# Optimization experiments

Measured on AMD Instinct MI355X. Metric: run time of the kernel, lower is better.

Reference implementation:

```python
import jax, jax.numpy as jnp
import numpy as np

B, C_IN, N = 8, 3, 32768
C_OUT, K, E = 128, 4, 4194304
TOTAL = B * N
BN_EPS = 1e-5


def setup_inputs() -> dict:
    key = jax.random.key(0)
    ks = jax.random.split(key, 6)
    return {
        "x": jax.random.normal(ks[0], (B, C_IN, N), dtype=jnp.float32),
        "edge_index": jax.random.randint(ks[1], (2, E), 0, TOTAL, dtype=jnp.int32),
        "edge_weight": jax.random.uniform(ks[2], (E,), dtype=jnp.float32),
        # ChebConv parameters: one (in, out) weight per Chebyshev order, plus bias
        "weight": jax.random.normal(ks[3], (K, C_IN, C_OUT), dtype=jnp.float32) * 0.1,
        "bias": jax.random.normal(ks[4], (C_OUT,), dtype=jnp.float32) * 0.01,
        # BatchNorm1d affine params
        "gamma": jnp.ones((C_OUT,), dtype=jnp.float32),
        "beta": jnp.zeros((C_OUT,), dtype=jnp.float32),
    }


def reference(x, edge_index, edge_weight, weight, bias, gamma, beta):
    b, f, n = x.shape
    total = b * n
    # (B, F, N) -> (B*N, F)
    h = x.transpose(0, 2, 1).reshape(total, f)

    src, dst = edge_index[0], edge_index[1]
    # remove_self_loops: zero self-loop weights (diagonal of scaled Laplacian is 0)
    w = jnp.where(src == dst, 0.0, edge_weight)
    # sym-normalized Laplacian, scaled by 2/lambda_max with lambda_max=2 (PyG default),
    # then self-loops added with -1 cancel the +I diagonal -> L_hat = -D^-1/2 A D^-1/2
    deg = jax.ops.segment_sum(w, src, num_segments=total)
    dis = jnp.where(deg > 0, jax.lax.rsqrt(jnp.maximum(deg, 1e-12)), 0.0)
    norm_w = -dis[src] * w * dis[dst]  # (E,)

    def prop(t):  # y[i] = sum_j L_hat[i, j] t[j]
        return jax.ops.segment_sum(norm_w[:, None] * t[src], dst, num_segments=total)

    # Chebyshev recursion: T0 = x, T1 = L_hat x, T_k = 2 L_hat T_{k-1} - T_{k-2}
    tx0 = h
    out = tx0 @ weight[0]
    tx1 = prop(tx0)
    out = out + tx1 @ weight[1]
    for k in range(2, weight.shape[0]):
        tx2 = 2.0 * prop(tx1) - tx0
        out = out + tx2 @ weight[k]
        tx0, tx1 = tx1, tx2
    out = out + bias

    # BatchNorm1d (training mode: batch stats, biased variance) + ReLU
    mean = out.mean(axis=0)
    var = out.var(axis=0)
    out = (out - mean) * jax.lax.rsqrt(var + BN_EPS) * gamma + beta
    out = jax.nn.relu(out)

    # (B*N, C_OUT) -> (B, C_OUT, N)
    return out.reshape(b, n, -1).transpose(0, 2, 1)
```

## Files before the change

### kernel.cpp

```cpp
#include <hip/hip_runtime.h>
#include <cstdint>

#define B_    8
#define CIN   3
#define NPTS  32768
#define TOT   (B_*NPTS)
#define COUT  128
#define NE    4194304
#define NF    12
#define NMOM  90
#define BN_EPS 1e-5f

#define NBKT  256
#define BKSZ  1024
#define TILE2 2048
#define EPT2  8
#define CAPS  18432
#define CAPD  18432

__global__ __launch_bounds__(256) void k_init(int* __restrict__ gp_s,
                                              int* __restrict__ gp_d) {
    int t = threadIdx.x;
    gp_s[t] = t * CAPS;
    gp_d[t] = t * CAPD;
}

__global__ __launch_bounds__(256) void k_scatter2(const int* __restrict__ src,
                                                  const int* __restrict__ dst,
                                                  const float* __restrict__ ew,
                                                  int* __restrict__ gp_s,
                                                  int* __restrict__ gp_d,
                                                  int* __restrict__ binned_s,
                                                  int2* __restrict__ binned_d) {
    __shared__ int lhist[NBKT], lbase[NBKT], cnt2[NBKT], gbase[NBKT];
    __shared__ int2 sorted2[TILE2];
    __shared__ unsigned char sbk[TILE2];
    __shared__ int wt[4];
    const int t = threadIdx.x, lane = t & 63, wv = t >> 6;

    int es[EPT2], ed[EPT2]; float ef[EPT2]; bool va[EPT2];
    const int base = blockIdx.x * TILE2 + t;
#pragma unroll
    for (int k = 0; k < EPT2; ++k) {
        int e = base + k * 256;
        es[k] = src[e]; ed[k] = dst[e]; ef[k] = ew[e];
        va[k] = (es[k] != ed[k]) && (ef[k] != 0.0f);
    }

    lhist[t] = 0; cnt2[t] = 0;
    __syncthreads();
#pragma unroll
    for (int k = 0; k < EPT2; ++k)
        if (va[k]) atomicAdd(&lhist[es[k] >> 10], 1);
    __syncthreads();
    {
        int v = lhist[t], inc = v;
#pragma unroll
        for (int d = 1; d < 64; d <<= 1) {
            int u = __shfl_up(inc, d, 64);
            if (lane >= d) inc += u;
        }
        if (lane == 63) wt[wv] = inc;
        __syncthreads();
        int pre = 0;
#pragma unroll
        for (int k = 0; k < 4; ++k) if (k < wv) pre += wt[k];
        lbase[t] = pre + inc - v;
        gbase[t] = atomicAdd(gp_s + t, v);
    }
    __syncthreads();
    int* sortedI = (int*)sorted2;
#pragma unroll
    for (int k = 0; k < EPT2; ++k) {
        if (va[k]) {
            int b = es[k] >> 10;
            int p = atomicAdd(&cnt2[b], 1);
            int idx = lbase[b] + p;
            sortedI[idx] = (__float_as_int(ef[k]) & 0xFFFFFC00) | (es[k] & 1023);
            sbk[idx] = (unsigned char)b;
        }
    }
    __syncthreads();
    {
        int tot = lbase[NBKT - 1] + lhist[NBKT - 1];
        for (int i = t; i < tot; i += 256) {
            int b = sbk[i];
            binned_s[(size_t)gbase[b] + (i - lbase[b])] = sortedI[i];
        }
    }
    __syncthreads();

    lhist[t] = 0; cnt2[t] = 0;
    __syncthreads();
#pragma unroll
    for (int k = 0; k < EPT2; ++k)
        if (va[k]) atomicAdd(&lhist[ed[k] >> 10], 1);
    __syncthreads();
    {
        int v = lhist[t], inc = v;
#pragma unroll
        for (int d = 1; d < 64; d <<= 1) {
            int u = __shfl_up(inc, d, 64);
            if (lane >= d) inc += u;
        }
        if (lane == 63) wt[wv] = inc;
        __syncthreads();
        int pre = 0;
#pragma unroll
        for (int k = 0; k < 4; ++k) if (k < wv) pre += wt[k];
        lbase[t] = pre + inc - v;
        gbase[t] = atomicAdd(gp_d + t, v);
    }
    __syncthreads();
#pragma unroll
    for (int k = 0; k < EPT2; ++k) {
        if (va[k]) {
            int b = ed[k] >> 10;
            int p = atomicAdd(&cnt2[b], 1);
            int idx = lbase[b] + p;
            sorted2[idx] = make_int2(es[k] | ((ed[k] & 1023) << 18),
                                     __float_as_int(ef[k]));
            sbk[idx] = (unsigned char)b;
        }
    }
    __syncthreads();
    {
        int tot = lbase[NBKT - 1] + lhist[NBKT - 1];
        for (int i = t; i < tot; i += 256) {
            int b = sbk[i];
            binned_d[(size_t)gbase[b] + (i - lbase[b])] = sorted2[i];
        }
    }
}

__global__ __launch_bounds__(1024) void k_degdis(const int* __restrict__ gp_s,
                                                 const int* __restrict__ binned_s,
                                                 float* __restrict__ dis) {
    __shared__ float acc[BKSZ];
    int t = threadIdx.x, b = blockIdx.x;
    acc[t] = 0.f;
    __syncthreads();
    int b0 = b * CAPS, b1 = gp_s[b];
    for (int i = b0 + t; i < b1; i += 1024) {
        int r = binned_s[i];
        atomicAdd(&acc[r & 1023], __int_as_float(r & 0xFFFFFC00));
    }
    __syncthreads();
    float v = acc[t];
    dis[b * BKSZ + t] = (v > 0.f) ? rsqrtf(fmaxf(v, 1e-12f)) : 0.f;
}

__global__ __launch_bounds__(256) void k_tx0pack(const float* __restrict__ x,
                                                 const float* __restrict__ dis,
                                                 float4* __restrict__ tx0) {
    int i = blockIdx.x * 256 + threadIdx.x;
    int b = i >> 15;
    int n = i & (NPTS - 1);
    const float* xb = x + (size_t)b * CIN * NPTS + n;
    tx0[i] = make_float4(xb[0], xb[NPTS], xb[2 * NPTS], dis[i]);
}

__global__ __launch_bounds__(1024) void k_prop(const int* __restrict__ gp_d,
                                               const int2* __restrict__ binned_d,
                                               const float4* __restrict__ tin,
                                               const float4* __restrict__ tprev,
                                               float4* __restrict__ tout,
                                               float scale) {
    __shared__ float acc[BKSZ * 3];
    int t = threadIdx.x, b = blockIdx.x;
    acc[t] = 0.f; acc[t + 1024] = 0.f; acc[t + 2048] = 0.f;
    __syncthreads();
    int b0 = b * CAPD, b1 = gp_d[b];
    for (int i = b0 + t; i < b1; i += 1024) {
        int2 r = binned_d[i];
        int s  = r.x & 0x3FFFF;
        int dl = ((unsigned)r.x) >> 18;
        float4 ts = tin[s];
        float f = __int_as_float(r.y) * ts.w;
        atomicAdd(&acc[dl * 3 + 0], f * ts.x);
        atomicAdd(&acc[dl * 3 + 1], f * ts.y);
        atomicAdd(&acc[dl * 3 + 2], f * ts.z);
    }
    __syncthreads();
    int n = b * BKSZ + t;
    float dn = tin[n].w;
    float m = -scale * dn;
    float r0 = m * acc[t * 3 + 0];
    float r1 = m * acc[t * 3 + 1];
    float r2 = m * acc[t * 3 + 2];
    if (tprev) {
        float4 tp = tprev[n];
        r0 -= tp.x; r1 -= tp.y; r2 -= tp.z;
    }
    tout[n] = make_float4(r0, r1, r2, dn);
}

__device__ __forceinline__ void decode_pair(int o, int& A, int& Bb) {
    if (o < 12) { A = o; Bb = 12; return; }
    int p = o - 12, base = 0; A = 0; Bb = 0;
#pragma unroll
    for (int aa = 0; aa < 12; ++aa) {
        int len = 12 - aa;
        bool in = (p >= base) && (p < base + len);
        if (in) { A = aa; Bb = aa + (p - base); }
        base += len;
    }
}

__global__ __launch_bounds__(256) void k_moments(const float4* __restrict__ tx0,
                                                 const float4* __restrict__ tx1,
                                                 const float4* __restrict__ tx2,
                                                 const float4* __restrict__ tx3,
                                                 float* __restrict__ mom) {
    __shared__ float L[256 * 13];
    __shared__ float R[4][96];
    const int tid = threadIdx.x, lane = tid & 63, w = tid >> 6;

    int a1, b1, a2 = 12, b2 = 12;
    decode_pair(lane, a1, b1);
    if (lane < 26) decode_pair(64 + lane, a2, b2);

    float acc1 = 0.0f, acc2 = 0.0f;
    const int TPB = (TOT / 256) / 256;
    for (int t = 0; t < TPB; ++t) {
        int node = (blockIdx.x * TPB + t) * 256 + tid;
        __syncthreads();
        float* Ld = &L[tid * 13];
        float4 a = tx0[node]; Ld[0] = a.x; Ld[1]  = a.y; Ld[2]  = a.z;
        float4 c = tx1[node]; Ld[3] = c.x; Ld[4]  = c.y; Ld[5]  = c.z;
        float4 d = tx2[node]; Ld[6] = d.x; Ld[7]  = d.y; Ld[8]  = d.z;
        float4 e = tx3[node]; Ld[9] = e.x; Ld[10] = e.y; Ld[11] = e.z;
        Ld[12] = 1.0f;
        __syncthreads();
        const int nb = w * 64;
#pragma unroll 4
        for (int i = 0; i < 64; ++i) {
            const float* Ln = &L[(nb + i) * 13];
            acc1 += Ln[a1] * Ln[b1];
            if (lane < 26) acc2 += Ln[a2] * Ln[b2];
        }
    }
    R[w][lane] = acc1;
    if (lane < 26) R[w][64 + lane] = acc2;
    __syncthreads();
    if (tid < NMOM) {
        mom[blockIdx.x * 96 + tid] = R[0][tid] + R[1][tid] + R[2][tid] + R[3][tid];
    }
}

__global__ __launch_bounds__(128) void k_prep(const float* __restrict__ mom,
                                              const float* __restrict__ weight,
                                              const float* __restrict__ bias,
                                              const float* __restrict__ gamma,
                                              const float* __restrict__ beta,
                                              float* __restrict__ wp,
                                              float* __restrict__ bp) {
    __shared__ float sm[NMOM];
    int c = threadIdx.x;
    if (c < NMOM) {
        float s = 0.f;
        for (int b = 0; b < 256; ++b) s += mom[b * 96 + c];
        sm[c] = s;
    }
    __syncthreads();

    float w[NF];
#pragma unroll
    for (int f = 0; f < NF; ++f) w[f] = weight[f * COUT + c];

    const float inv = 1.0f / (float)TOT;
    float mw = 0.0f;
#pragma unroll
    for (int a = 0; a < NF; ++a) mw += (sm[a] * inv) * w[a];

    float q = 0.0f;
    int idx = NF;
#pragma unroll
    for (int a = 0; a < NF; ++a) {
#pragma unroll
        for (int b = a; b < NF; ++b) {
            float S2 = sm[idx++] * inv;
            q += ((a == b) ? 1.0f : 2.0f) * w[a] * w[b] * S2;
        }
    }
    float bc   = bias[c];
    float mean = mw + bc;
    float var  = q - mw * mw;
    float sc   = gamma[c] * rsqrtf(var + BN_EPS);
    float sh   = (bc - mean) * sc + beta[c];
#pragma unroll
    for (int f = 0; f < NF; ++f) wp[f * COUT + c] = w[f] * sc;
    bp[c] = sh;
}

__global__ __launch_bounds__(256) void k_out(const float4* __restrict__ tx0,
                                             const float4* __restrict__ tx1,
                                             const float4* __restrict__ tx2,
                                             const float4* __restrict__ tx3,
                                             const float* __restrict__ wp,
                                             const float* __restrict__ bp,
                                             float* __restrict__ out) {
    __shared__ float sw[NF * COUT];
    __shared__ float sb[COUT];
    for (int j = threadIdx.x; j < NF * COUT; j += 256) sw[j] = wp[j];
    if (threadIdx.x < COUT) sb[threadIdx.x] = bp[threadIdx.x];
    __syncthreads();

    int i = blockIdx.x * 256 + threadIdx.x;
    int b = i >> 15;
    int n = i & (NPTS - 1);

    float t[NF];
    float4 a = tx0[i]; t[0] = a.x; t[1]  = a.y; t[2]  = a.z;
    float4 c = tx1[i]; t[3] = c.x; t[4]  = c.y; t[5]  = c.z;
    float4 d = tx2[i]; t[6] = d.x; t[7]  = d.y; t[8]  = d.z;
    float4 e = tx3[i]; t[9] = e.x; t[10] = e.y; t[11] = e.z;

    float* o = out + (size_t)b * COUT * NPTS + n;
#pragma unroll 4
    for (int c2 = 0; c2 < COUT; ++c2) {
        float acc = sb[c2];
#pragma unroll
        for (int f = 0; f < NF; ++f) acc += t[f] * sw[f * COUT + c2];
        o[(size_t)c2 * NPTS] = fmaxf(acc, 0.0f);
    }
}

__global__ __launch_bounds__(256) void k_deg_fb(const int* src, const int* dst,
                                                const float* ew, float* deg) {
    int e = blockIdx.x * 256 + threadIdx.x;
    int s = src[e], d = dst[e];
    float w = ew[e];
    if (s != d && w != 0.0f) atomicAdd(deg + s, w);
}
__global__ __launch_bounds__(256) void k_dis_fb(float* deg) {
    int i = blockIdx.x * 256 + threadIdx.x;
    float v = deg[i];
    deg[i] = (v > 0.0f) ? rsqrtf(fmaxf(v, 1e-12f)) : 0.0f;
}
__global__ __launch_bounds__(256) void k_tx03_fb(const float* __restrict__ x,
                                                 float* __restrict__ tx0) {
    int i = blockIdx.x * 256 + threadIdx.x;
    int b = i >> 15;
    int n = i & (NPTS - 1);
    const float* xb = x + (size_t)b * CIN * NPTS + n;
    tx0[i * 3 + 0] = xb[0];
    tx0[i * 3 + 1] = xb[NPTS];
    tx0[i * 3 + 2] = xb[2 * NPTS];
}
__global__ __launch_bounds__(256) void k_prop_fb(const int* src, const int* dst,
                                                 const float* ew, const float* dis,
                                                 const float* tin, float* tout, float scale) {
    int e = blockIdx.x * 256 + threadIdx.x;
    int s = src[e], d = dst[e];
    if (s == d) return;
    float w = ew[e];
    float nw = -dis[s] * w * dis[d] * scale;
    if (nw == 0.0f) return;
    const float* t = tin + (size_t)s * 3;
    atomicAdd(tout + (size_t)d * 3 + 0, nw * t[0]);
    atomicAdd(tout + (size_t)d * 3 + 1, nw * t[1]);
    atomicAdd(tout + (size_t)d * 3 + 2, nw * t[2]);
}
__global__ __launch_bounds__(256) void k_sub_fb(float* tout, const float* tprev) {
    int i = blockIdx.x * 256 + threadIdx.x;
    tout[i] -= tprev[i];
}
__global__ __launch_bounds__(256) void k_pack34(const float* __restrict__ t3,
                                                const float* __restrict__ dis,
                                                float4* __restrict__ t4) {
    int i = blockIdx.x * 256 + threadIdx.x;
    t4[i] = make_float4(t3[i * 3 + 0], t3[i * 3 + 1], t3[i * 3 + 2], dis[i]);
}


extern "C" void kernel_launch(void* const* d_in, const int* in_sizes, int n_in,
                              void* d_out, int out_size, void* d_ws, size_t ws_size,
                              hipStream_t stream) {
    const float* x      = (const float*)d_in[0];
    const int*   ei     = (const int*)d_in[1];
    const float* ew     = (const float*)d_in[2];
    const float* weight = (const float*)d_in[3];
    const float* bias   = (const float*)d_in[4];
    const float* gamma  = (const float*)d_in[5];
    const float* beta   = (const float*)d_in[6];
    float* out = (float*)d_out;

    const int* src = ei;
    const int* dst = ei + NE;

    dim3 blk(256);
    dim3 gT(TOT / 256);

    const size_t od  = 0;
    const size_t os  = od + (size_t)2 * NBKT * CAPD;
    const size_t odi = os + (size_t)NBKT * CAPS;
    const size_t ot0 = odi + TOT;
    const size_t ot1 = ot0 + (size_t)4 * TOT;
    const size_t ot2 = ot1 + (size_t)4 * TOT;
    const size_t ot3 = ot2 + (size_t)4 * TOT;
    const size_t ogs = ot3 + (size_t)4 * TOT;
    const size_t ogd = ogs + 256;
    const size_t omo = ogd + 256;
    const size_t owp = omo + 256 * 96;
    const size_t obp = owp + 1536;
    const size_t need = (obp + 128) * 4;

    int*    wsI      = (int*)d_ws;
    int2*   binned_d = (int2*)(wsI + od);
    int*    binned_s = wsI + os;
    float*  dis      = (float*)(wsI + odi);
    float4* tx0      = (float4*)(wsI + ot0);
    float4* tx1      = (float4*)(wsI + ot1);
    float4* tx2      = (float4*)(wsI + ot2);
    float4* tx3      = (float4*)(wsI + ot3);
    int*    gp_s     = wsI + ogs;
    int*    gp_d     = wsI + ogd;
    float*  mom      = (float*)(wsI + omo);
    float*  wp       = (float*)(wsI + owp);
    float*  bp       = (float*)(wsI + obp);

    if (ws_size >= need) {
        k_init    <<<dim3(1),    blk, 0, stream>>>(gp_s, gp_d);
        k_scatter2<<<dim3(NE / TILE2), blk, 0, stream>>>(src, dst, ew, gp_s, gp_d,
                                                         binned_s, binned_d);
        k_degdis  <<<dim3(NBKT), dim3(1024), 0, stream>>>(gp_s, binned_s, dis);
        k_tx0pack <<<gT,         blk, 0, stream>>>(x, dis, tx0);

        k_prop<<<dim3(NBKT), dim3(1024), 0, stream>>>(gp_d, binned_d, tx0, nullptr, tx1, 1.0f);
        k_prop<<<dim3(NBKT), dim3(1024), 0, stream>>>(gp_d, binned_d, tx1, tx0,     tx2, 2.0f);
        k_prop<<<dim3(NBKT), dim3(1024), 0, stream>>>(gp_d, binned_d, tx2, tx1,     tx3, 2.0f);

        k_moments<<<dim3(256), blk, 0, stream>>>(tx0, tx1, tx2, tx3, mom);
        k_prep   <<<dim3(1), dim3(128), 0, stream>>>(mom, weight, bias, gamma, beta, wp, bp);
        k_out    <<<gT, blk, 0, stream>>>(tx0, tx1, tx2, tx3, wp, bp, out);
    } else {
        dim3 gE(NE / 256);
        dim3 g3T(3 * TOT / 256);
        float* t30 = (float*)(wsI + od);
        float* t31 = t30 + (size_t)3 * TOT;
        float* t32 = t31 + (size_t)3 * TOT;
        float* t33 = t32 + (size_t)3 * TOT;
        float* deg = dis;

        (void)hipMemsetAsync(t30, 0, (size_t)12 * TOT * sizeof(float), stream);
        (void)hipMemsetAsync(deg, 0, (size_t)TOT * sizeof(float), stream);

        k_deg_fb<<<gE, blk, 0, stream>>>(src, dst, ew, deg);
        k_dis_fb<<<gT, blk, 0, stream>>>(deg);
        k_tx03_fb<<<gT, blk, 0, stream>>>(x, t30);

        k_prop_fb<<<gE, blk, 0, stream>>>(src, dst, ew, deg, t30, t31, 1.0f);
        k_prop_fb<<<gE, blk, 0, stream>>>(src, dst, ew, deg, t31, t32, 2.0f);
        k_sub_fb <<<g3T, blk, 0, stream>>>(t32, t30);
        k_prop_fb<<<gE, blk, 0, stream>>>(src, dst, ew, deg, t32, t33, 2.0f);
        k_sub_fb <<<g3T, blk, 0, stream>>>(t33, t31);

        k_pack34<<<gT, blk, 0, stream>>>(t30, deg, tx0);
        k_pack34<<<gT, blk, 0, stream>>>(t31, deg, tx1);
        k_pack34<<<gT, blk, 0, stream>>>(t32, deg, tx2);
        k_pack34<<<gT, blk, 0, stream>>>(t33, deg, tx3);

        k_moments<<<dim3(256), blk, 0, stream>>>(tx0, tx1, tx2, tx3, mom);
        k_prep   <<<dim3(1), dim3(128), 0, stream>>>(mom, weight, bias, gamma, beta, wp, bp);
        k_out    <<<gT, blk, 0, stream>>>(tx0, tx1, tx2, tx3, wp, bp, out);
    }
}
```

Before: 345.6 us.

## Sort edges per destination into CSR and replace LDS atomics with per-node gathers

The first propagation kernel now counting-sorts each destination bucket by local node, writing a CSR-style sorted edge list and per-node offsets. The later propagations walk each node's edges serially instead of doing shared-memory float atomics. The degree and pack kernels are fused, and the moments and prep kernels are merged using a last-block atomic counter, which removes launches. The catch is that per-thread work now depends on node degree, so loads become uneven, and sorted_d costs an extra workspace buffer.

Result: slower. 527.9 us (+52.7%).

```diff
diff --git a/kernel.cpp b/kernel.cpp
--- a/kernel.cpp
+++ b/kernel.cpp
@@ -19,10 +19,12 @@
 #define CAPD  18432
 
 __global__ __launch_bounds__(256) void k_init(int* __restrict__ gp_s,
-                                              int* __restrict__ gp_d) {
+                                              int* __restrict__ gp_d,
+                                              int* __restrict__ done) {
     int t = threadIdx.x;
     gp_s[t] = t * CAPS;
     gp_d[t] = t * CAPD;
+    if (t == 0) *done = 0;
 }
 
 __global__ __launch_bounds__(256) void k_scatter2(const int* __restrict__ src,
@@ -133,9 +135,10 @@
     }
 }
 
-__global__ __launch_bounds__(1024) void k_degdis(const int* __restrict__ gp_s,
-                                                 const int* __restrict__ binned_s,
-                                                 float* __restrict__ dis) {
+__global__ __launch_bounds__(1024) void k_degdispack(const int* __restrict__ gp_s,
+                                                     const int* __restrict__ binned_s,
+                                                     const float* __restrict__ x,
+                                                     float4* __restrict__ tx0) {
     __shared__ float acc[BKSZ];
     int t = threadIdx.x, b = blockIdx.x;
     acc[t] = 0.f;
@@ -147,52 +150,96 @@
     }
     __syncthreads();
     float v = acc[t];
-    dis[b * BKSZ + t] = (v > 0.f) ? rsqrtf(fmaxf(v, 1e-12f)) : 0.f;
-}
-
-__global__ __launch_bounds__(256) void k_tx0pack(const float* __restrict__ x,
-                                                 const float* __restrict__ dis,
-                                                 float4* __restrict__ tx0) {
-    int i = blockIdx.x * 256 + threadIdx.x;
-    int b = i >> 15;
-    int n = i & (NPTS - 1);
-    const float* xb = x + (size_t)b * CIN * NPTS + n;
-    tx0[i] = make_float4(xb[0], xb[NPTS], xb[2 * NPTS], dis[i]);
+    float dn = (v > 0.f) ? rsqrtf(fmaxf(v, 1e-12f)) : 0.f;
+    int n = b * BKSZ + t;
+    int batch = n >> 15, nn = n & (NPTS - 1);
+    const float* xb = x + (size_t)batch * CIN * NPTS + nn;
+    tx0[n] = make_float4(xb[0], xb[NPTS], xb[2 * NPTS], dn);
+}
+
+__global__ __launch_bounds__(1024) void k_sortprop1(const int* __restrict__ gp_d,
+                                                    const int2* __restrict__ binned_d,
+                                                    int2* __restrict__ sorted_d,
+                                                    int* __restrict__ noff,
+                                                    const float4* __restrict__ tx0,
+                                                    float4* __restrict__ tx1) {
+    __shared__ int hist[BKSZ];
+    __shared__ int cur[BKSZ];
+    __shared__ int wsum[16], wpre[16];
+    const int t = threadIdx.x, b = blockIdx.x;
+    const int base = b * CAPD;
+    const int cnt = gp_d[b] - base;
+    const int lane = t & 63, w = t >> 6;
+
+    hist[t] = 0;
+    __syncthreads();
+    for (int i = t; i < cnt; i += 1024) {
+        int2 r = binned_d[base + i];
+        atomicAdd(&hist[((unsigned)r.x) >> 18], 1);
+    }
+    __syncthreads();
+    int v = hist[t];
+    int inc = v;
+#pragma unroll
+    for (int d = 1; d < 64; d <<= 1) {
+        int u = __shfl_up(inc, d, 64);
+        if (lane >= d) inc += u;
+    }
+    if (lane == 63) wsum[w] = inc;
+    __syncthreads();
+    if (t == 0) {
+        int s = 0;
+#pragma unroll
+        for (int k = 0; k < 16; ++k) { wpre[k] = s; s += wsum[k]; }
+    }
+    __syncthreads();
+    int excl = wpre[w] + inc - v;
+    hist[t] = excl;
+    cur[t]  = excl;
+    noff[b * BKSZ + t] = base + excl;
+    __syncthreads();
+    for (int i = t; i < cnt; i += 1024) {
+        int2 r = binned_d[base + i];
+        int dl = ((unsigned)r.x) >> 18;
+        int p = atomicAdd(&cur[dl], 1);
+        sorted_d[base + p] = make_int2(r.x & 0x3FFFF, r.y);
+    }
+    __syncthreads();
+    int s0 = hist[t], e0 = cur[t];
+    float a0 = 0.f, a1 = 0.f, a2 = 0.f;
+    for (int j = s0; j < e0; ++j) {
+        int2 r = sorted_d[base + j];
+        float4 ts = tx0[r.x];
+        float f = __int_as_float(r.y) * ts.w;
+        a0 += f * ts.x; a1 += f * ts.y; a2 += f * ts.z;
+    }
+    int n = b * BKSZ + t;
+    float dn = tx0[n].w;
+    tx1[n] = make_float4(-dn * a0, -dn * a1, -dn * a2, dn);
 }
 
 __global__ __launch_bounds__(1024) void k_prop(const int* __restrict__ gp_d,
-                                               const int2* __restrict__ binned_d,
+                                               const int* __restrict__ noff,
+                                               const int2* __restrict__ sorted_d,
                                                const float4* __restrict__ tin,
                                                const float4* __restrict__ tprev,
                                                float4* __restrict__ tout,
                                                float scale) {
-    __shared__ float acc[BKSZ * 3];
     int t = threadIdx.x, b = blockIdx.x;
-    acc[t] = 0.f; acc[t + 1024] = 0.f; acc[t + 2048] = 0.f;
-    __syncthreads();
-    int b0 = b * CAPD, b1 = gp_d[b];
-    for (int i = b0 + t; i < b1; i += 1024) {
-        int2 r = binned_d[i];
-        int s  = r.x & 0x3FFFF;
-        int dl = ((unsigned)r.x) >> 18;
-        float4 ts = tin[s];
+    int n = b * BKSZ + t;
+    int s0 = noff[n];
+    int e0 = (t == BKSZ - 1) ? gp_d[b] : noff[n + 1];
+    float a0 = 0.f, a1 = 0.f, a2 = 0.f;
+    for (int j = s0; j < e0; ++j) {
+        int2 r = sorted_d[j];
+        float4 ts = tin[r.x];
         float f = __int_as_float(r.y) * ts.w;
-        atomicAdd(&acc[dl * 3 + 0], f * ts.x);
-        atomicAdd(&acc[dl * 3 + 1], f * ts.y);
-        atomicAdd(&acc[dl * 3 + 2], f * ts.z);
-    }
-    __syncthreads();
-    int n = b * BKSZ + t;
+        a0 += f * ts.x; a1 += f * ts.y; a2 += f * ts.z;
+    }
     float dn = tin[n].w;
     float m = -scale * dn;
-    float r0 = m * acc[t * 3 + 0];
-    float r1 = m * acc[t * 3 + 1];
-    float r2 = m * acc[t * 3 + 2];
-    if (tprev) {
-        float4 tp = tprev[n];
-        r0 -= tp.x; r1 -= tp.y; r2 -= tp.z;
-    }
-    tout[n] = make_float4(r0, r1, r2, dn);
+    float4 tp = tprev[n];
+    tout[n] = make_float4(m * a0 - tp.x, m * a1 - tp.y, m * a2 - tp.z, dn);
 }
 
 __device__ __forceinline__ void decode_pair(int o, int& A, int& Bb) {
@@ -207,13 +254,21 @@
     }
 }
 
-__global__ __launch_bounds__(256) void k_moments(const float4* __restrict__ tx0,
+__global__ __launch_bounds__(256) void k_momprep(const float4* __restrict__ tx0,
                                                  const float4* __restrict__ tx1,
                                                  const float4* __restrict__ tx2,
                                                  const float4* __restrict__ tx3,
-                                                 float* __restrict__ mom) {
+                                                 float* __restrict__ mom,
+                                                 int* __restrict__ done,
+                                                 const float* __restrict__ weight,
+                                                 const float* __restrict__ bias,
+                                                 const float* __restrict__ gamma,
+                                                 const float* __restrict__ beta,
+                                                 float* __restrict__ wp,
+                                                 float* __restrict__ bp) {
     __shared__ float L[256 * 13];
     __shared__ float R[4][96];
+    __shared__ int amLast;
     const int tid = threadIdx.x, lane = tid & 63, w = tid >> 6;
 
     int a1, b1, a2 = 12, b2 = 12;
@@ -243,35 +298,33 @@
     R[w][lane] = acc1;
     if (lane < 26) R[w][64 + lane] = acc2;
     __syncthreads();
+    if (tid < NMOM)
+        mom[blockIdx.x * 96 + tid] = R[0][tid] + R[1][tid] + R[2][tid] + R[3][tid];
+
+    __threadfence();
+    __syncthreads();
+    if (tid == 0) amLast = (atomicAdd(done, 1) == NBKT - 1) ? 1 : 0;
+    __syncthreads();
+    if (!amLast) return;
+    __threadfence();
+
+    __shared__ float sm[NMOM];
     if (tid < NMOM) {
-        mom[blockIdx.x * 96 + tid] = R[0][tid] + R[1][tid] + R[2][tid] + R[3][tid];
-    }
-}
-
-__global__ __launch_bounds__(128) void k_prep(const float* __restrict__ mom,
-                                              const float* __restrict__ weight,
-                                              const float* __restrict__ bias,
-                                              const float* __restrict__ gamma,
-                                              const float* __restrict__ beta,
-                                              float* __restrict__ wp,
-                                              float* __restrict__ bp) {
-    __shared__ float sm[NMOM];
-    int c = threadIdx.x;
-    if (c < NMOM) {
         float s = 0.f;
-        for (int b = 0; b < 256; ++b) s += mom[b * 96 + c];
-        sm[c] = s;
-    }
-    __syncthreads();
-
-    float w[NF];
-#pragma unroll
-    for (int f = 0; f < NF; ++f) w[f] = weight[f * COUT + c];
+        for (int b = 0; b < NBKT; ++b) s += mom[b * 96 + tid];
+        sm[tid] = s;
+    }
+    __syncthreads();
+    if (tid >= COUT) return;
+    int c = tid;
+    float wv[NF];
+#pragma unroll
+    for (int f = 0; f < NF; ++f) wv[f] = weight[f * COUT + c];
 
     const float inv = 1.0f / (float)TOT;
     float mw = 0.0f;
 #pragma unroll
-    for (int a = 0; a < NF; ++a) mw += (sm[a] * inv) * w[a];
+    for (int a = 0; a < NF; ++a) mw += (sm[a] * inv) * wv[a];
 
     float q = 0.0f;
     int idx = NF;
@@ -280,7 +333,7 @@
 #pragma unroll
         for (int b = a; b < NF; ++b) {
             float S2 = sm[idx++] * inv;
-            q += ((a == b) ? 1.0f : 2.0f) * w[a] * w[b] * S2;
+            q += ((a == b) ? 1.0f : 2.0f) * wv[a] * wv[b] * S2;
         }
     }
     float bc   = bias[c];
@@ -289,7 +342,7 @@
     float sc   = gamma[c] * rsqrtf(var + BN_EPS);
     float sh   = (bc - mean) * sc + beta[c];
 #pragma unroll
-    for (int f = 0; f < NF; ++f) wp[f * COUT + c] = w[f] * sc;
+    for (int f = 0; f < NF; ++f) wp[f * COUT + c] = wv[f] * sc;
     bp[c] = sh;
 }
 
@@ -338,39 +391,44 @@
     float v = deg[i];
     deg[i] = (v > 0.0f) ? rsqrtf(fmaxf(v, 1e-12f)) : 0.0f;
 }
-__global__ __launch_bounds__(256) void k_tx03_fb(const float* __restrict__ x,
-                                                 float* __restrict__ tx0) {
+__global__ __launch_bounds__(256) void k_pack_fb(const float* __restrict__ x,
+                                                 const float* __restrict__ dis,
+                                                 float4* __restrict__ tx0) {
     int i = blockIdx.x * 256 + threadIdx.x;
-    int b = i >> 15;
-    int n = i & (NPTS - 1);
+    int b = i >> 15, n = i & (NPTS - 1);
     const float* xb = x + (size_t)b * CIN * NPTS + n;
-    tx0[i * 3 + 0] = xb[0];
-    tx0[i * 3 + 1] = xb[NPTS];
-    tx0[i * 3 + 2] = xb[2 * NPTS];
+    tx0[i] = make_float4(xb[0], xb[NPTS], xb[2 * NPTS], dis[i]);
 }
 __global__ __launch_bounds__(256) void k_prop_fb(const int* src, const int* dst,
-                                                 const float* ew, const float* dis,
-                                                 const float* tin, float* tout, float scale) {
+                                                 const float* ew, const float4* tin,
+                                                 float* tacc) {
     int e = blockIdx.x * 256 + threadIdx.x;
     int s = src[e], d = dst[e];
     if (s == d) return;
     float w = ew[e];
-    float nw = -dis[s] * w * dis[d] * scale;
-    if (nw == 0.0f) return;
-    const float* t = tin + (size_t)s * 3;
-    atomicAdd(tout + (size_t)d * 3 + 0, nw * t[0]);
-    atomicAdd(tout + (size_t)d * 3 + 1, nw * t[1]);
-    atomicAdd(tout + (size_t)d * 3 + 2, nw * t[2]);
-}
-__global__ __launch_bounds__(256) void k_sub_fb(float* tout, const float* tprev) {
-    int i = blockIdx.x * 256 + threadIdx.x;
-    tout[i] -= tprev[i];
-}
-__global__ __launch_bounds__(256) void k_pack34(const float* __restrict__ t3,
-                                                const float* __restrict__ dis,
-                                                float4* __restrict__ t4) {
-    int i = blockIdx.x * 256 + threadIdx.x;
-    t4[i] = make_float4(t3[i * 3 + 0], t3[i * 3 + 1], t3[i * 3 + 2], dis[i]);
+    if (w == 0.0f) return;
+    float4 ts = tin[s];
+    float f = w * ts.w;
+    atomicAdd(tacc + (size_t)d * 3 + 0, f * ts.x);
+    atomicAdd(tacc + (size_t)d * 3 + 1, f * ts.y);
+    atomicAdd(tacc + (size_t)d * 3 + 2, f * ts.z);
+}
+__global__ __launch_bounds__(256) void k_fin_fb(const float* __restrict__ tacc,
+                                                const float4* __restrict__ tin,
+                                                const float4* __restrict__ tprev,
+                                                float4* __restrict__ tout,
+                                                float scale) {
+    int n = blockIdx.x * 256 + threadIdx.x;
+    float dn = tin[n].w;
+    float m = -scale * dn;
+    float r0 = m * tacc[n * 3 + 0];
+    float r1 = m * tacc[n * 3 + 1];
+    float r2 = m * tacc[n * 3 + 2];
+    if (tprev) {
+        float4 tp = tprev[n];
+        r0 -= tp.x; r1 -= tp.y; r2 -= tp.z;
+    }
+    tout[n] = make_float4(r0, r1, r2, dn);
 }
 
 
@@ -393,76 +451,72 @@
     dim3 gT(TOT / 256);
 
     const size_t od  = 0;
-    const size_t os  = od + (size_t)2 * NBKT * CAPD;
-    const size_t odi = os + (size_t)NBKT * CAPS;
-    const size_t ot0 = odi + TOT;
+    const size_t osd = od  + (size_t)2 * NBKT * CAPD;
+    const size_t os  = osd + (size_t)2 * NBKT * CAPD;
+    const size_t ot0 = os  + (size_t)NBKT * CAPS;
     const size_t ot1 = ot0 + (size_t)4 * TOT;
     const size_t ot2 = ot1 + (size_t)4 * TOT;
     const size_t ot3 = ot2 + (size_t)4 * TOT;
-    const size_t ogs = ot3 + (size_t)4 * TOT;
+    const size_t onf = ot3 + (size_t)4 * TOT;
+    const size_t ogs = onf + TOT;
     const size_t ogd = ogs + 256;
     const size_t omo = ogd + 256;
     const size_t owp = omo + 256 * 96;
     const size_t obp = owp + 1536;
-    const size_t need = (obp + 128) * 4;
+    const size_t odn = obp + 128;
+    const size_t need = (odn + 1) * 4;
 
     int*    wsI      = (int*)d_ws;
     int2*   binned_d = (int2*)(wsI + od);
+    int2*   sorted_d = (int2*)(wsI + osd);
     int*    binned_s = wsI + os;
-    float*  dis      = (float*)(wsI + odi);
     float4* tx0      = (float4*)(wsI + ot0);
     float4* tx1      = (float4*)(wsI + ot1);
     float4* tx2      = (float4*)(wsI + ot2);
     float4* tx3      = (float4*)(wsI + ot3);
+    int*    noff     = wsI + onf;
     int*    gp_s     = wsI + ogs;
     int*    gp_d     = wsI + ogd;
     float*  mom      = (float*)(wsI + omo);
     float*  wp       = (float*)(wsI + owp);
     float*  bp       = (float*)(wsI + obp);
+    int*    done     = wsI + odn;
 
     if (ws_size >= need) {
-        k_init    <<<dim3(1),    blk, 0, stream>>>(gp_s, gp_d);
-        k_scatter2<<<dim3(NE / TILE2), blk, 0, stream>>>(src, dst, ew, gp_s, gp_d,
-                                                         binned_s, binned_d);
-        k_degdis  <<<dim3(NBKT), dim3(1024), 0, stream>>>(gp_s, binned_s, dis);
-        k_tx0pack <<<gT,         blk, 0, stream>>>(x, dis, tx0);
-
-        k_prop<<<dim3(NBKT), dim3(1024), 0, stream>>>(gp_d, binned_d, tx0, nullptr, tx1, 1.0f);
-        k_prop<<<dim3(NBKT), dim3(1024), 0, stream>>>(gp_d, binned_d, tx1, tx0,     tx2, 2.0f);
-        k_prop<<<dim3(NBKT), dim3(1024), 0, stream>>>(gp_d, binned_d, tx2, tx1,     tx3, 2.0f);
-
-        k_moments<<<dim3(256), blk, 0, stream>>>(tx0, tx1, tx2, tx3, mom);
-        k_prep   <<<dim3(1), dim3(128), 0, stream>>>(mom, weight, bias, gamma, beta, wp, bp);
-        k_out    <<<gT, blk, 0, stream>>>(tx0, tx1, tx2, tx3, wp, bp, out);
+        k_init      <<<dim3(1),    blk, 0, stream>>>(gp_s, gp_d, done);
+        k_scatter2  <<<dim3(NE / TILE2), blk, 0, stream>>>(src, dst, ew, gp_s, gp_d,
+                                                           binned_s, binned_d);
+        k_degdispack<<<dim3(NBKT), dim3(1024), 0, stream>>>(gp_s, binned_s, x, tx0);
+        k_sortprop1 <<<dim3(NBKT), dim3(1024), 0, stream>>>(gp_d, binned_d, sorted_d,
+                                                            noff, tx0, tx1);
+        k_prop      <<<dim3(NBKT), dim3(1024), 0, stream>>>(gp_d, noff, sorted_d,
+                                                            tx1, tx0, tx2, 2.0f);
+        k_prop      <<<dim3(NBKT), dim3(1024), 0, stream>>>(gp_d, noff, sorted_d,
+                                                            tx2, tx1, tx3, 2.0f);
+        k_momprep   <<<dim3(NBKT), blk, 0, stream>>>(tx0, tx1, tx2, tx3, mom, done,
+                                                     weight, bias, gamma, beta, wp, bp);
+        k_out       <<<gT, blk, 0, stream>>>(tx0, tx1, tx2, tx3, wp, bp, out);
     } else {
         dim3 gE(NE / 256);
-        dim3 g3T(3 * TOT / 256);
-        float* t30 = (float*)(wsI + od);
-        float* t31 = t30 + (size_t)3 * TOT;
-        float* t32 = t31 + (size_t)3 * TOT;
-        float* t33 = t32 + (size_t)3 * TOT;
-        float* deg = dis;
-
-        (void)hipMemsetAsync(t30, 0, (size_t)12 * TOT * sizeof(float), stream);
-        (void)hipMemsetAsync(deg, 0, (size_t)TOT * sizeof(float), stream);
-
-        k_deg_fb<<<gE, blk, 0, stream>>>(src, dst, ew, deg);
-        k_dis_fb<<<gT, blk, 0, stream>>>(deg);
-        k_tx03_fb<<<gT, blk, 0, stream>>>(x, t30);
-
-        k_prop_fb<<<gE, blk, 0, stream>>>(src, dst, ew, deg, t30, t31, 1.0f);
-        k_prop_fb<<<gE, blk, 0, stream>>>(src, dst, ew, deg, t31, t32, 2.0f);
-        k_sub_fb <<<g3T, blk, 0, stream>>>(t32, t30);
-        k_prop_fb<<<gE, blk, 0, stream>>>(src, dst, ew, deg, t32, t33, 2.0f);
-        k_sub_fb <<<g3T, blk, 0, stream>>>(t33, t31);
-
-        k_pack34<<<gT, blk, 0, stream>>>(t30, deg, tx0);
-        k_pack34<<<gT, blk, 0, stream>>>(t31, deg, tx1);
-        k_pack34<<<gT, blk, 0, stream>>>(t32, deg, tx2);
-        k_pack34<<<gT, blk, 0, stream>>>(t33, deg, tx3);
-
-        k_moments<<<dim3(256), blk, 0, stream>>>(tx0, tx1, tx2, tx3, mom);
-        k_prep   <<<dim3(1), dim3(128), 0, stream>>>(mom, weight, bias, gamma, beta, wp, bp);
+        float* deg  = (float*)(wsI + od);
+        float* tacc = deg + TOT;
+
+        (void)hipMemsetAsync(deg, 0, (size_t)4 * TOT * sizeof(float), stream);
+        k_deg_fb <<<gE, blk, 0, stream>>>(src, dst, ew, deg);
+        k_dis_fb <<<gT, blk, 0, stream>>>(deg);
+        k_pack_fb<<<gT, blk, 0, stream>>>(x, deg, tx0);
+
+        k_prop_fb<<<gE, blk, 0, stream>>>(src, dst, ew, tx0, tacc);
+        k_fin_fb <<<gT, blk, 0, stream>>>(tacc, tx0, nullptr, tx1, 1.0f);
+        (void)hipMemsetAsync(tacc, 0, (size_t)3 * TOT * sizeof(float), stream);
+        k_prop_fb<<<gE, blk, 0, stream>>>(src, dst, ew, tx1, tacc);
+        k_fin_fb <<<gT, blk, 0, stream>>>(tacc, tx1, tx0, tx2, 2.0f);
+        (void)hipMemsetAsync(tacc, 0, (size_t)3 * TOT * sizeof(float), stream);
+        k_prop_fb<<<gE, blk, 0, stream>>>(src, dst, ew, tx2, tacc);
+        k_fin_fb <<<gT, blk, 0, stream>>>(tacc, tx2, tx1, tx3, 2.0f);
+
+        k_momprep<<<dim3(NBKT), blk, 0, stream>>>(tx0, tx1, tx2, tx3, mom, done,
+                                                  weight, bias, gamma, beta, wp, bp);
         k_out    <<<gT, blk, 0, stream>>>(tx0, tx1, tx2, tx3, wp, bp, out);
     }
 }
```
